# Optimization experiments

Hardware: AMD Instinct MI355X
Metric: run time of the kernel (lower is better)

## Reference

```python
import jax, jax.numpy as jnp
import numpy as np
import math
from jax import lax

B, L = 64, 8192
S = L // 8          # width after 3 stride-(1,2) SAME convs
D = 4 * 5           # height(4) * channels(5) -> per-token feature dim
D_FLAT = S * D


def setup_inputs():
    key = jax.random.key(0)
    ks = jax.random.split(key, 32)
    sc = 0.1
    inp = {
        "inputs": jax.random.randint(ks[0], (B, L), 0, 4, dtype=jnp.int32),
        # conv stack: HWIO kernels, Conv2D(5,(4,4),(1,2),'SAME')
        "conv_w1": sc * jax.random.normal(ks[1], (4, 4, 1, 5), jnp.float32),
        "conv_b1": jnp.zeros((5,), jnp.float32),
        "conv_w2": sc * jax.random.normal(ks[2], (4, 4, 5, 5), jnp.float32),
        "conv_b2": jnp.zeros((5,), jnp.float32),
        "conv_w3": sc * jax.random.normal(ks[3], (4, 4, 5, 5), jnp.float32),
        "conv_b3": jnp.zeros((5,), jnp.float32),
        # 3 SelfAttn blocks, each with K/Q/V projections [D, D]
        "attn1_K": sc * jax.random.normal(ks[4], (D, D), jnp.float32),
        "attn1_Q": sc * jax.random.normal(ks[5], (D, D), jnp.float32),
        "attn1_V": sc * jax.random.normal(ks[6], (D, D), jnp.float32),
        "attn2_K": sc * jax.random.normal(ks[7], (D, D), jnp.float32),
        "attn2_Q": sc * jax.random.normal(ks[8], (D, D), jnp.float32),
        "attn2_V": sc * jax.random.normal(ks[9], (D, D), jnp.float32),
        "attn3_K": sc * jax.random.normal(ks[10], (D, D), jnp.float32),
        "attn3_Q": sc * jax.random.normal(ks[11], (D, D), jnp.float32),
        "attn3_V": sc * jax.random.normal(ks[12], (D, D), jnp.float32),
        # 3 Dense(10) layers (no activation, as in Keras defaults)
        "dense_w1": 0.01 * jax.random.normal(ks[13], (D_FLAT, 10), jnp.float32),
        "dense_b1": jnp.zeros((10,), jnp.float32),
        "dense_w2": sc * jax.random.normal(ks[14], (10, 10), jnp.float32),
        "dense_b2": jnp.zeros((10,), jnp.float32),
        "dense_w3": sc * jax.random.normal(ks[15], (10, 10), jnp.float32),
        "dense_b3": jnp.zeros((10,), jnp.float32),
    }
    return inp


def _conv(x, w, b):
    # NHWC, HWIO, strides (1,2), SAME
    y = lax.conv_general_dilated(x, w, window_strides=(1, 2), padding="SAME",
                                 dimension_numbers=("NHWC", "HWIO", "NHWC"))
    return y + b


def _self_attn(x, Kw, Qw, Vw):
    # x: [B, S, D]; manual causal scaled dot-product attention
    K = x @ Kw
    Q = x @ Qw
    V = x @ Vw
    s = Q.shape[1]
    mask = jnp.triu(jnp.full((s, s), -jnp.inf, dtype=x.dtype), k=1)
    scores = jnp.einsum("bsd,btd->bst", Q, K) / math.sqrt(K.shape[-1]) + mask
    return jax.nn.softmax(scores, axis=-1) @ V


def reference(inputs, conv_w1, conv_b1, conv_w2, conv_b2, conv_w3, conv_b3,
              attn1_K, attn1_Q, attn1_V, attn2_K, attn2_Q, attn2_V,
              attn3_K, attn3_Q, attn3_V,
              dense_w1, dense_b1, dense_w2, dense_b2, dense_w3, dense_b3):
    # one_hot over axis=1 -> [B, 4, L], then channel dim -> [B, 4, L, 1]
    x = jax.nn.one_hot(inputs, 4, axis=1, dtype=jnp.float32)[..., None]
    x = _conv(x, conv_w1, conv_b1)
    x = _conv(x, conv_w2, conv_b2)
    x = _conv(x, conv_w3, conv_b3)            # [B, 4, S, 5]
    # tokens along width, features = height(4) x channels(5)
    x = jnp.transpose(x, (0, 2, 1, 3)).reshape(x.shape[0], S, D)
    x = _self_attn(x, attn1_K, attn1_Q, attn1_V)
    x = _self_attn(x, attn2_K, attn2_Q, attn2_V)
    x = _self_attn(x, attn3_K, attn3_Q, attn3_V)
    x = x.reshape(x.shape[0], -1)             # flatten [B, S*D]
    x = x @ dense_w1 + dense_b1
    x = x @ dense_w2 + dense_b2
    x = x @ dense_w3 + dense_b3               # [B, 10]
    return x
```

## Files before the change

kernel.cpp:

```cpp
#include <hip/hip_runtime.h>
#include <hip/hip_bf16.h>


#define B_ 64
#define L_ 8192
#define S_ 1024
#define D_ 20

typedef unsigned short ushort_t;
typedef __attribute__((ext_vector_type(8))) short short8_t;
typedef __attribute__((ext_vector_type(4))) short short4_t;
typedef __attribute__((ext_vector_type(4))) float f32x4_t;

__device__ __forceinline__ ushort_t f2bf(float f) {
  unsigned u = __float_as_uint(f);
  return (ushort_t)((u + 0x7fffu + ((u >> 16) & 1u)) >> 16);
}
__device__ __forceinline__ float bf2f(ushort_t h) {
  return __uint_as_float(((unsigned)h) << 16);
}

__global__ __launch_bounds__(256) void conv12_kernel(
    const int* __restrict__ inp,
    const float* __restrict__ W1c, const float* __restrict__ B1c,
    const float* __restrict__ W2c, const float* __restrict__ B2c,
    float* __restrict__ out,
    const float* __restrict__ W1d,
    float* __restrict__ W1T) {
  __shared__ float w1s[80], b1s[5], w2s[400], b2s[5];
  for (int j = threadIdx.x; j < 400; j += 256) w2s[j] = W2c[j];
  if (threadIdx.x < 80)      w1s[threadIdx.x]      = W1c[threadIdx.x];
  else if (threadIdx.x < 85) b1s[threadIdx.x - 80] = B1c[threadIdx.x - 80];
  else if (threadIdx.x < 90) b2s[threadIdx.x - 85] = B2c[threadIdx.x - 85];
  __syncthreads();
  const int idx = blockIdx.x * 256 + threadIdx.x;
  const int b  = idx >> 11;
  const int wo = idx & 2047;
  const int* ib = inp + (size_t)b * L_;
  int iv[10];
#pragma unroll
  for (int t = 0; t < 10; ++t) {
    int g = 4 * wo - 3 + t;
    iv[t] = (g >= 0 && g < L_) ? ib[g] : -100;
  }
  float val[4][4][5];
#pragma unroll
  for (int pos = 0; pos < 4; ++pos) {
    const int w1 = 2 * wo - 1 + pos;
    const bool okp = (w1 >= 0 && w1 < 4096);
#pragma unroll
    for (int hi = 0; hi < 4; ++hi)
#pragma unroll
      for (int ci = 0; ci < 5; ++ci) val[hi][pos][ci] = okp ? b1s[ci] : 0.f;
    if (okp) {
#pragma unroll
      for (int kw = 0; kw < 4; ++kw) {
        const int gw = 2 * w1 - 1 + kw;
        if (gw >= 0 && gw < L_) {
          const int v = iv[2 * pos + kw];
#pragma unroll
          for (int hi = 0; hi < 4; ++hi) {
            const int kh = v - hi + 1;
            if (kh >= 0 && kh < 4) {
#pragma unroll
              for (int ci = 0; ci < 5; ++ci)
                val[hi][pos][ci] += w1s[(kh * 4 + kw) * 5 + ci];
            }
          }
        }
      }
    }
  }
  float acc[4][5];
#pragma unroll
  for (int h = 0; h < 4; ++h)
#pragma unroll
    for (int c = 0; c < 5; ++c) acc[h][c] = b2s[c];
#pragma unroll
  for (int kh = 0; kh < 4; ++kh)
#pragma unroll
    for (int kw = 0; kw < 4; ++kw)
#pragma unroll
      for (int ci = 0; ci < 5; ++ci) {
        const float* wp = w2s + ((kh * 4 + kw) * 5 + ci) * 5;
        float w0 = wp[0], w1v = wp[1], w2v = wp[2], w3 = wp[3], w4 = wp[4];
#pragma unroll
        for (int h = 0; h < 4; ++h) {
          int hi = h - 1 + kh;
          if (hi >= 0 && hi < 4) {
            float x = val[hi][kw][ci];
            acc[h][0] += w0 * x;  acc[h][1] += w1v * x; acc[h][2] += w2v * x;
            acc[h][3] += w3 * x;  acc[h][4] += w4 * x;
          }
        }
      }
  float* ob = out + (size_t)b * 4 * 2048 * 5;
#pragma unroll
  for (int h = 0; h < 4; ++h)
#pragma unroll
    for (int c = 0; c < 5; ++c) ob[(h * 2048 + wo) * 5 + c] = acc[h][c];
  for (int j = idx; j < 204800; j += 131072) {
    int col = j / 20480, i2 = j - col * 20480;
    W1T[j] = W1d[i2 * 10 + col];
  }
}

__global__ __launch_bounds__(256) void conv3_proj_kernel(
    const float* __restrict__ in,
    const float* __restrict__ W,  const float* __restrict__ Bi,
    const float* __restrict__ Kw, const float* __restrict__ Qw,
    const float* __restrict__ Vw,
    ushort_t* __restrict__ Qb, ushort_t* __restrict__ Kb,
    ushort_t* __restrict__ Vf) {
  constexpr int WIN = 2048;
  __shared__ float ws[400], bs[5];
  __shared__ float kw[400], qw[400], vw[400];
  for (int j = threadIdx.x; j < 400; j += 256) {
    ws[j] = W[j]; kw[j] = Kw[j]; qw[j] = Qw[j]; vw[j] = Vw[j];
  }
  if (threadIdx.x < 5) bs[threadIdx.x] = Bi[threadIdx.x];
  __syncthreads();
  const int r  = blockIdx.x * 256 + threadIdx.x;
  const int b  = r >> 10;
  const int wo = r & 1023;
  float val[4][4][5];
#pragma unroll
  for (int hi = 0; hi < 4; ++hi) {
    const float* ir = in + ((size_t)b * 4 + hi) * WIN * 5;
#pragma unroll
    for (int kwp = 0; kwp < 4; ++kwp) {
      int wi = 2 * wo - 1 + kwp;
      bool ok = (wi >= 0 && wi < WIN);
#pragma unroll
      for (int ci = 0; ci < 5; ++ci) val[hi][kwp][ci] = ok ? ir[wi * 5 + ci] : 0.f;
    }
  }
  float acc[4][5];
#pragma unroll
  for (int h = 0; h < 4; ++h)
#pragma unroll
    for (int c = 0; c < 5; ++c) acc[h][c] = bs[c];
#pragma unroll
  for (int kh = 0; kh < 4; ++kh)
#pragma unroll
    for (int kwp = 0; kwp < 4; ++kwp)
#pragma unroll
      for (int ci = 0; ci < 5; ++ci) {
        const float* wp = ws + ((kh * 4 + kwp) * 5 + ci) * 5;
        float w0 = wp[0], w1 = wp[1], w2 = wp[2], w3 = wp[3], w4 = wp[4];
#pragma unroll
        for (int h = 0; h < 4; ++h) {
          int hi = h - 1 + kh;
          if (hi >= 0 && hi < 4) {
            float x = val[hi][kwp][ci];
            acc[h][0] += w0 * x; acc[h][1] += w1 * x; acc[h][2] += w2 * x;
            acc[h][3] += w3 * x; acc[h][4] += w4 * x;
          }
        }
      }
  float x[D_];
#pragma unroll
  for (int h = 0; h < 4; ++h)
#pragma unroll
    for (int c = 0; c < 5; ++c) x[h * 5 + c] = acc[h][c];
  float q[D_], k[D_], v[D_];
#pragma unroll
  for (int j = 0; j < D_; ++j) { q[j] = 0.f; k[j] = 0.f; v[j] = 0.f; }
#pragma unroll
  for (int i = 0; i < D_; ++i) {
#pragma unroll
    for (int j = 0; j < D_; ++j) {
      q[j] += x[i] * qw[i * D_ + j];
      k[j] += x[i] * kw[i * D_ + j];
      v[j] += x[i] * vw[i * D_ + j];
    }
  }
  const float sc = 0.22360679774997896f;
  ushort_t qt[32], kt[32];
#pragma unroll
  for (int j = 0; j < D_; ++j) { qt[j] = f2bf(q[j] * sc); kt[j] = f2bf(k[j]); }
#pragma unroll
  for (int j = D_; j < 32; ++j) { qt[j] = 0; kt[j] = 0; }
  int4* qd = (int4*)(Qb + (size_t)r * 32);
  int4* kd = (int4*)(Kb + (size_t)r * 32);
#pragma unroll
  for (int j = 0; j < 4; ++j) {
    qd[j] = *(const int4*)(qt + 8 * j);
    kd[j] = *(const int4*)(kt + 8 * j);
  }
  ushort_t* vbase = Vf + ((size_t)b * 64 + (wo >> 4)) * 320 + (wo & 15);
#pragma unroll
  for (int d = 0; d < D_; ++d) vbase[d * 16] = f2bf(v[d]);
}

template <bool FUSE>
__global__ __launch_bounds__(512, 8) void attn_kernel(
    const ushort_t* __restrict__ Qb, const ushort_t* __restrict__ Kb,
    const ushort_t* __restrict__ Vf,
    const float* __restrict__ Kw2, const float* __restrict__ Qw2,
    const float* __restrict__ Vw2,
    ushort_t* __restrict__ Qb2, ushort_t* __restrict__ Kb2,
    ushort_t* __restrict__ Vf2,
    const float* __restrict__ W1T,
    float* __restrict__ part2) {
  __shared__ float ox[1280];
  __shared__ float pw_s[FUSE ? 1200 : 4];
  __shared__ float mrgL[64];
  __shared__ float red2[40];
  const int blk   = blockIdx.x;
  const int b     = blk & 63;
  const int raw   = blk >> 6;
  const int rr4   = raw & 3, k4 = raw >> 2;
  const int strip = (k4 == 0) ? rr4 : (k4 == 1) ? 7 - rr4
                  : (k4 == 2) ? 8 + rr4 : 15 - rr4;
  const int q0    = strip * 64;
  const int nt    = q0 + 64;
  const int tid   = threadIdx.x;
  const int w     = tid >> 6;
  const int sub   = w & 3;
  const int half  = w >> 2;
  const int lane  = tid & 63;
  const int n     = lane & 15;
  const int quad  = lane >> 4;
  const int qbase = q0 + 16 * sub;
  const int qg    = qbase + n;
  if (FUSE) {
    for (int j = tid; j < 1200; j += 512) {
      int m = j / 400, oo = j - m * 400;
      pw_s[j] = (m == 0) ? Kw2[oo] : (m == 1) ? Qw2[oo] : Vw2[oo];
    }
  }
  const ushort_t* KbB  = Kb + (size_t)b * 1024 * 32;
  const ushort_t* VfB  = Vf + (size_t)b * 20480;
  const ushort_t* vloB = VfB + n * 16 + quad * 4;
  const ushort_t* vhiB = VfB + (16 + (n & 3)) * 16 + quad * 4;
  short8_t qfrag = *(const short8_t*)(Qb + ((size_t)(b * 1024 + qbase + n)) * 32 + quad * 8);
  f32x4_t oA = {0.f, 0.f, 0.f, 0.f};
  f32x4_t oB = {0.f, 0.f, 0.f, 0.f};
  const f32x4_t zero = {0.f, 0.f, 0.f, 0.f};
  float lsum = 0.f;
  const int nt2 = nt >> 1;
  const int tlo = half ? nt2 : 0;
  int thi = half ? nt : nt2;
  if (thi > qbase + 16) thi = qbase + 16;
  for (int t0 = tlo; t0 < thi; t0 += 32) {
    short8_t kf0 = *(const short8_t*)(KbB + (size_t)(t0 + n) * 32 + quad * 8);
    short8_t kf1 = *(const short8_t*)(KbB + (size_t)(t0 + 16 + n) * 32 + quad * 8);
#pragma unroll
    for (int c = 0; c < 2; ++c) {
      const int tg = t0 + c * 16 + quad * 4;
      f32x4_t s = __builtin_amdgcn_mfma_f32_16x16x32_bf16(c ? kf1 : kf0, qfrag,
                                                          zero, 0, 0, 0);
      ushort_t pk4[4];
#pragma unroll
      for (int r = 0; r < 4; ++r) {
        float p = (tg + r <= qg) ? __expf(s[r]) : 0.f;
        ushort_t h = f2bf(p);
        lsum += bf2f(h);
        pk4[r] = h;
      }
      short4_t pfrag = *(const short4_t*)pk4;
      const int tb = (t0 >> 4) + c;
      short4_t vlo = *(const short4_t*)(vloB + tb * 320);
      short4_t vhi = *(const short4_t*)(vhiB + tb * 320);
      oA = __builtin_amdgcn_mfma_f32_16x16x16bf16_1k(vlo, pfrag, oA, 0, 0, 0);
      oB = __builtin_amdgcn_mfma_f32_16x16x16bf16_1k(vhi, pfrag, oB, 0, 0, 0);
    }
  }
  float l = lsum;
  l += __shfl_xor(l, 16, 64);
  l += __shfl_xor(l, 32, 64);
  float* oxw = ox + sub * 320;
  if (half) {
#pragma unroll
    for (int r = 0; r < 4; ++r) oxw[n * 20 + quad * 4 + r] = oA[r];
    if (quad == 0) {
#pragma unroll
      for (int r = 0; r < 4; ++r) oxw[n * 20 + 16 + r] = oB[r];
      mrgL[sub * 16 + n] = l;
    }
  }
  __syncthreads();
  if (!half) {
#pragma unroll
    for (int r = 0; r < 4; ++r) oA[r] += oxw[n * 20 + quad * 4 + r];
    if (quad == 0) {
#pragma unroll
      for (int r = 0; r < 4; ++r) oB[r] += oxw[n * 20 + 16 + r];
    }
    l += mrgL[sub * 16 + n];
    const float inv = 1.f / l;
#pragma unroll
    for (int r = 0; r < 4; ++r) oxw[n * 20 + quad * 4 + r] = oA[r] * inv;
    if (quad == 0) {
#pragma unroll
      for (int r = 0; r < 4; ++r) oxw[n * 20 + 16 + r] = oB[r] * inv;
    }
  }
  if (FUSE) {
    if (!half) {
      __asm__ volatile("s_waitcnt lgkmcnt(0)" ::: "memory");
      const int row  = lane >> 2;
      const int part = lane & 3;
      float x[D_];
#pragma unroll
      for (int i = 0; i < D_; ++i) x[i] = oxw[row * 20 + i];
      float qv[5], kv[5], vv[5];
#pragma unroll
      for (int jj = 0; jj < 5; ++jj) { qv[jj] = 0.f; kv[jj] = 0.f; vv[jj] = 0.f; }
#pragma unroll
      for (int i = 0; i < D_; ++i) {
        const float xi = x[i];
#pragma unroll
        for (int jj = 0; jj < 5; ++jj) {
          const int j = 5 * part + jj;
          kv[jj] += xi * pw_s[i * 20 + j];
          qv[jj] += xi * pw_s[400 + i * 20 + j];
          vv[jj] += xi * pw_s[800 + i * 20 + j];
        }
      }
      const float sc = 0.22360679774997896f;
      const int rg = b * 1024 + qbase + row;
      const int s  = rg & 1023;
#pragma unroll
      for (int jj = 0; jj < 5; ++jj) {
        const int j = 5 * part + jj;
        Kb2[(size_t)rg * 32 + j] = f2bf(kv[jj]);
        Qb2[(size_t)rg * 32 + j] = f2bf(qv[jj] * sc);
        Vf2[(size_t)b * 20480 + (size_t)(s >> 4) * 320 + j * 16 + (s & 15)] =
            f2bf(vv[jj]);
      }
      if (part == 0) {
#pragma unroll
        for (int u = 0; u < 6; ++u)
          *(unsigned*)(Kb2 + (size_t)rg * 32 + 20 + 2 * u) = 0u;
      } else if (part == 1) {
#pragma unroll
        for (int u = 0; u < 6; ++u)
          *(unsigned*)(Qb2 + (size_t)rg * 32 + 20 + 2 * u) = 0u;
      }
    }
  } else {
    __syncthreads();
    float acc[10];
#pragma unroll
    for (int j = 0; j < 10; ++j) acc[j] = 0.f;
    const int base = q0 * 20;
    if (tid < 256) {
#pragma unroll
      for (int k = 0; k < 5; ++k) {
        const int il = tid + 256 * k;
        const float xv = ox[il];
#pragma unroll
        for (int j = 0; j < 10; ++j)
          acc[j] += xv * W1T[(size_t)j * 20480 + base + il];
      }
    }
#pragma unroll
    for (int off = 1; off < 64; off <<= 1) {
#pragma unroll
      for (int j = 0; j < 10; ++j) acc[j] += __shfl_xor(acc[j], off, 64);
    }
    if (tid < 256 && lane == 0) {
#pragma unroll
      for (int j = 0; j < 10; ++j) red2[w * 10 + j] = acc[j];
    }
    __syncthreads();
    if (tid < 10) {
      float s2 = red2[tid] + red2[10 + tid] + red2[20 + tid] + red2[30 + tid];
      part2[((b << 4) + strip) * 10 + tid] = s2;
    }
  }
}

__global__ __launch_bounds__(64) void dense_final(
    const float* __restrict__ part2,
    const float* __restrict__ B1,
    const float* __restrict__ W2, const float* __restrict__ B2,
    const float* __restrict__ W3, const float* __restrict__ B3,
    float* __restrict__ out) {
  const int b = blockIdx.x;
  __shared__ float y1[10], y2[10];
  if (threadIdx.x < 10) {
    int j = threadIdx.x;
    float s = 0.f;
#pragma unroll
    for (int st = 0; st < 16; ++st) s += part2[((b << 4) + st) * 10 + j];
    y1[j] = s + B1[j];
  }
  __syncthreads();
  if (threadIdx.x < 10) {
    int j = threadIdx.x;
    float s = B2[j];
#pragma unroll
    for (int i = 0; i < 10; ++i) s += y1[i] * W2[i * 10 + j];
    y2[j] = s;
  }
  __syncthreads();
  if (threadIdx.x < 10) {
    int j = threadIdx.x;
    float s = B3[j];
#pragma unroll
    for (int i = 0; i < 10; ++i) s += y2[i] * W3[i * 10 + j];
    out[b * 10 + j] = s;
  }
}

extern "C" void kernel_launch(void* const* d_in, const int* in_sizes, int n_in,
                              void* d_out, int out_size, void* d_ws, size_t ws_size,
                              hipStream_t stream) {
  const int*   inp = (const int*)d_in[0];
  const float* cw1 = (const float*)d_in[1];
  const float* cb1 = (const float*)d_in[2];
  const float* cw2 = (const float*)d_in[3];
  const float* cb2 = (const float*)d_in[4];
  const float* cw3 = (const float*)d_in[5];
  const float* cb3 = (const float*)d_in[6];
  const float* a1K = (const float*)d_in[7];
  const float* a1Q = (const float*)d_in[8];
  const float* a1V = (const float*)d_in[9];
  const float* a2K = (const float*)d_in[10];
  const float* a2Q = (const float*)d_in[11];
  const float* a2V = (const float*)d_in[12];
  const float* a3K = (const float*)d_in[13];
  const float* a3Q = (const float*)d_in[14];
  const float* a3V = (const float*)d_in[15];
  const float* dw1 = (const float*)d_in[16];
  const float* db1 = (const float*)d_in[17];
  const float* dw2 = (const float*)d_in[18];
  const float* db2 = (const float*)d_in[19];
  const float* dw3 = (const float*)d_in[20];
  const float* db3 = (const float*)d_in[21];
  float* outp = (float*)d_out;

  float* wsf = (float*)d_ws;
  ushort_t* qbA  = (ushort_t*)(wsf);
  ushort_t* kbA  = (ushort_t*)(wsf + 1048576);
  ushort_t* vfA  = (ushort_t*)(wsf + 2097152);
  float*    part2= wsf + 4456448;
  float*    w1t  = wsf + 4466688;
  ushort_t* qbB  = (ushort_t*)(wsf + 4671488);
  ushort_t* kbB  = (ushort_t*)(wsf + 5712384);
  ushort_t* vfB  = (ushort_t*)(wsf + 6760960);
  float*    c2   = wsf + 5242880;

  conv12_kernel<<<512, 256, 0, stream>>>(inp, cw1, cb1, cw2, cb2, c2, dw1, w1t);

  conv3_proj_kernel<<<256, 256, 0, stream>>>(c2, cw3, cb3, a1K, a1Q, a1V, qbA, kbA, vfA);
  attn_kernel<true><<<1024, 512, 0, stream>>>(
      qbA, kbA, vfA, a2K, a2Q, a2V, qbB, kbB, vfB, nullptr, nullptr);
  attn_kernel<true><<<1024, 512, 0, stream>>>(
      qbB, kbB, vfB, a3K, a3Q, a3V, qbA, kbA, vfA, nullptr, nullptr);
  attn_kernel<false><<<1024, 512, 0, stream>>>(
      qbA, kbA, vfA, nullptr, nullptr, nullptr, nullptr, nullptr, nullptr,
      w1t, part2);

  dense_final<<<64, 64, 0, stream>>>(part2, db1, dw2, db2, dw3, db3, outp);
}
```

Measured before the change: 199.2 us.

## Split conv kernels across four lanes per output with shuffle reduction

Result: no change. 202.0 us (+1.4%).

```diff
diff --git a/kernel.cpp b/kernel.cpp
--- a/kernel.cpp
+++ b/kernel.cpp
@@ -33,75 +33,71 @@
   else if (threadIdx.x < 85) b1s[threadIdx.x - 80] = B1c[threadIdx.x - 80];
   else if (threadIdx.x < 90) b2s[threadIdx.x - 85] = B2c[threadIdx.x - 85];
   __syncthreads();
-  const int idx = blockIdx.x * 256 + threadIdx.x;
-  const int b  = idx >> 11;
-  const int wo = idx & 2047;
+  const int j   = blockIdx.x * 256 + threadIdx.x;
+  const int pos = j & 3;
+  const int idx = j >> 2;
+  const int b   = idx >> 11;
+  const int wo  = idx & 2047;
   const int* ib = inp + (size_t)b * L_;
-  int iv[10];
-#pragma unroll
-  for (int t = 0; t < 10; ++t) {
-    int g = 4 * wo - 3 + t;
-    iv[t] = (g >= 0 && g < L_) ? ib[g] : -100;
-  }
-  float val[4][4][5];
-#pragma unroll
-  for (int pos = 0; pos < 4; ++pos) {
-    const int w1 = 2 * wo - 1 + pos;
-    const bool okp = (w1 >= 0 && w1 < 4096);
-#pragma unroll
-    for (int hi = 0; hi < 4; ++hi)
-#pragma unroll
-      for (int ci = 0; ci < 5; ++ci) val[hi][pos][ci] = okp ? b1s[ci] : 0.f;
-    if (okp) {
-#pragma unroll
-      for (int kw = 0; kw < 4; ++kw) {
-        const int gw = 2 * w1 - 1 + kw;
-        if (gw >= 0 && gw < L_) {
-          const int v = iv[2 * pos + kw];
-#pragma unroll
-          for (int hi = 0; hi < 4; ++hi) {
-            const int kh = v - hi + 1;
-            if (kh >= 0 && kh < 4) {
-#pragma unroll
-              for (int ci = 0; ci < 5; ++ci)
-                val[hi][pos][ci] += w1s[(kh * 4 + kw) * 5 + ci];
-            }
+  float vp[4][5];
+  const int w1 = 2 * wo - 1 + pos;
+  const bool okp = (w1 >= 0 && w1 < 4096);
+#pragma unroll
+  for (int hi = 0; hi < 4; ++hi)
+#pragma unroll
+    for (int ci = 0; ci < 5; ++ci) vp[hi][ci] = okp ? b1s[ci] : 0.f;
+  if (okp) {
+#pragma unroll
+    for (int kw = 0; kw < 4; ++kw) {
+      const int gw = 2 * w1 - 1 + kw;
+      if (gw >= 0 && gw < L_) {
+        const int v = ib[gw];
+#pragma unroll
+        for (int hi = 0; hi < 4; ++hi) {
+          const int kh = v - hi + 1;
+          if (kh >= 0 && kh < 4) {
+#pragma unroll
+            for (int ci = 0; ci < 5; ++ci)
+              vp[hi][ci] += w1s[(kh * 4 + kw) * 5 + ci];
           }
         }
       }
     }
   }
-  float acc[4][5];
+  float part[4][5];
 #pragma unroll
   for (int h = 0; h < 4; ++h)
 #pragma unroll
-    for (int c = 0; c < 5; ++c) acc[h][c] = b2s[c];
+    for (int c = 0; c < 5; ++c) part[h][c] = 0.f;
 #pragma unroll
   for (int kh = 0; kh < 4; ++kh)
 #pragma unroll
-    for (int kw = 0; kw < 4; ++kw)
-#pragma unroll
-      for (int ci = 0; ci < 5; ++ci) {
-        const float* wp = w2s + ((kh * 4 + kw) * 5 + ci) * 5;
-        float w0 = wp[0], w1v = wp[1], w2v = wp[2], w3 = wp[3], w4 = wp[4];
-#pragma unroll
-        for (int h = 0; h < 4; ++h) {
-          int hi = h - 1 + kh;
-          if (hi >= 0 && hi < 4) {
-            float x = val[hi][kw][ci];
-            acc[h][0] += w0 * x;  acc[h][1] += w1v * x; acc[h][2] += w2v * x;
-            acc[h][3] += w3 * x;  acc[h][4] += w4 * x;
-          }
+    for (int ci = 0; ci < 5; ++ci) {
+      const float* wp = w2s + ((kh * 4 + pos) * 5 + ci) * 5;
+      float w0 = wp[0], w1v = wp[1], w2v = wp[2], w3v = wp[3], w4v = wp[4];
+#pragma unroll
+      for (int h = 0; h < 4; ++h) {
+        int hi = h - 1 + kh;
+        if (hi >= 0 && hi < 4) {
+          float x = vp[hi][ci];
+          part[h][0] += w0 * x;  part[h][1] += w1v * x; part[h][2] += w2v * x;
+          part[h][3] += w3v * x; part[h][4] += w4v * x;
         }
       }
+    }
+#pragma unroll
+  for (int m = 1; m <= 2; m <<= 1)
+#pragma unroll
+    for (int h = 0; h < 4; ++h)
+#pragma unroll
+      for (int c = 0; c < 5; ++c) part[h][c] += __shfl_xor(part[h][c], m, 64);
   float* ob = out + (size_t)b * 4 * 2048 * 5;
 #pragma unroll
-  for (int h = 0; h < 4; ++h)
-#pragma unroll
-    for (int c = 0; c < 5; ++c) ob[(h * 2048 + wo) * 5 + c] = acc[h][c];
-  for (int j = idx; j < 204800; j += 131072) {
-    int col = j / 20480, i2 = j - col * 20480;
-    W1T[j] = W1d[i2 * 10 + col];
+  for (int c = 0; c < 5; ++c)
+    ob[(pos * 2048 + wo) * 5 + c] = part[pos][c] + b2s[c];
+  for (int t = j; t < 204800; t += 524288) {
+    int col = t / 20480, i2 = t - col * 20480;
+    W1T[t] = W1d[i2 * 10 + col];
   }
 }
 
@@ -114,83 +110,90 @@
     ushort_t* __restrict__ Vf) {
   constexpr int WIN = 2048;
   __shared__ float ws[400], bs[5];
-  __shared__ float kw[400], qw[400], vw[400];
-  for (int j = threadIdx.x; j < 400; j += 256) {
-    ws[j] = W[j]; kw[j] = Kw[j]; qw[j] = Qw[j]; vw[j] = Vw[j];
+  __shared__ float kws[400], qws[400], vws[400];
+  for (int i = threadIdx.x; i < 400; i += 256) {
+    ws[i] = W[i]; kws[i] = Kw[i]; qws[i] = Qw[i]; vws[i] = Vw[i];
   }
   if (threadIdx.x < 5) bs[threadIdx.x] = Bi[threadIdx.x];
   __syncthreads();
-  const int r  = blockIdx.x * 256 + threadIdx.x;
+  const int j  = blockIdx.x * 256 + threadIdx.x;
+  const int p  = j & 3;
+  const int r  = j >> 2;
   const int b  = r >> 10;
   const int wo = r & 1023;
-  float val[4][4][5];
+  const int wi = 2 * wo - 1 + p;
+  const bool ok = (wi >= 0 && wi < WIN);
+  float vp[4][5];
 #pragma unroll
   for (int hi = 0; hi < 4; ++hi) {
     const float* ir = in + ((size_t)b * 4 + hi) * WIN * 5;
 #pragma unroll
-    for (int kwp = 0; kwp < 4; ++kwp) {
-      int wi = 2 * wo - 1 + kwp;
-      bool ok = (wi >= 0 && wi < WIN);
-#pragma unroll
-      for (int ci = 0; ci < 5; ++ci) val[hi][kwp][ci] = ok ? ir[wi * 5 + ci] : 0.f;
-    }
-  }
-  float acc[4][5];
+    for (int ci = 0; ci < 5; ++ci) vp[hi][ci] = ok ? ir[wi * 5 + ci] : 0.f;
+  }
+  float part[4][5];
 #pragma unroll
   for (int h = 0; h < 4; ++h)
 #pragma unroll
-    for (int c = 0; c < 5; ++c) acc[h][c] = bs[c];
+    for (int c = 0; c < 5; ++c) part[h][c] = 0.f;
 #pragma unroll
   for (int kh = 0; kh < 4; ++kh)
 #pragma unroll
-    for (int kwp = 0; kwp < 4; ++kwp)
-#pragma unroll
-      for (int ci = 0; ci < 5; ++ci) {
-        const float* wp = ws + ((kh * 4 + kwp) * 5 + ci) * 5;
-        float w0 = wp[0], w1 = wp[1], w2 = wp[2], w3 = wp[3], w4 = wp[4];
-#pragma unroll
-        for (int h = 0; h < 4; ++h) {
-          int hi = h - 1 + kh;
-          if (hi >= 0 && hi < 4) {
-            float x = val[hi][kwp][ci];
-            acc[h][0] += w0 * x; acc[h][1] += w1 * x; acc[h][2] += w2 * x;
-            acc[h][3] += w3 * x; acc[h][4] += w4 * x;
-          }
+    for (int ci = 0; ci < 5; ++ci) {
+      const float* wp = ws + ((kh * 4 + p) * 5 + ci) * 5;
+      float w0 = wp[0], w1 = wp[1], w2 = wp[2], w3 = wp[3], w4 = wp[4];
+#pragma unroll
+      for (int h = 0; h < 4; ++h) {
+        int hi = h - 1 + kh;
+        if (hi >= 0 && hi < 4) {
+          float x = vp[hi][ci];
+          part[h][0] += w0 * x; part[h][1] += w1 * x; part[h][2] += w2 * x;
+          part[h][3] += w3 * x; part[h][4] += w4 * x;
         }
       }
+    }
+#pragma unroll
+  for (int m = 1; m <= 2; m <<= 1)
+#pragma unroll
+    for (int h = 0; h < 4; ++h)
+#pragma unroll
+      for (int c = 0; c < 5; ++c) part[h][c] += __shfl_xor(part[h][c], m, 64);
   float x[D_];
 #pragma unroll
   for (int h = 0; h < 4; ++h)
 #pragma unroll
-    for (int c = 0; c < 5; ++c) x[h * 5 + c] = acc[h][c];
-  float q[D_], k[D_], v[D_];
-#pragma unroll
-  for (int j = 0; j < D_; ++j) { q[j] = 0.f; k[j] = 0.f; v[j] = 0.f; }
+    for (int c = 0; c < 5; ++c) x[h * 5 + c] = part[h][c] + bs[c];
+  float qv[5], kv[5], vv[5];
+#pragma unroll
+  for (int jj = 0; jj < 5; ++jj) { qv[jj] = 0.f; kv[jj] = 0.f; vv[jj] = 0.f; }
 #pragma unroll
   for (int i = 0; i < D_; ++i) {
-#pragma unroll
-    for (int j = 0; j < D_; ++j) {
-      q[j] += x[i] * qw[i * D_ + j];
-      k[j] += x[i] * kw[i * D_ + j];
-      v[j] += x[i] * vw[i * D_ + j];
+    const float xi = x[i];
+#pragma unroll
+    for (int jj = 0; jj < 5; ++jj) {
+      const int col = 5 * p + jj;
+      kv[jj] += xi * kws[i * D_ + col];
+      qv[jj] += xi * qws[i * D_ + col];
+      vv[jj] += xi * vws[i * D_ + col];
     }
   }
   const float sc = 0.22360679774997896f;
-  ushort_t qt[32], kt[32];
-#pragma unroll
-  for (int j = 0; j < D_; ++j) { qt[j] = f2bf(q[j] * sc); kt[j] = f2bf(k[j]); }
-#pragma unroll
-  for (int j = D_; j < 32; ++j) { qt[j] = 0; kt[j] = 0; }
-  int4* qd = (int4*)(Qb + (size_t)r * 32);
-  int4* kd = (int4*)(Kb + (size_t)r * 32);
-#pragma unroll
-  for (int j = 0; j < 4; ++j) {
-    qd[j] = *(const int4*)(qt + 8 * j);
-    kd[j] = *(const int4*)(kt + 8 * j);
-  }
-  ushort_t* vbase = Vf + ((size_t)b * 64 + (wo >> 4)) * 320 + (wo & 15);
-#pragma unroll
-  for (int d = 0; d < D_; ++d) vbase[d * 16] = f2bf(v[d]);
+#pragma unroll
+  for (int jj = 0; jj < 5; ++jj) {
+    const int col = 5 * p + jj;
+    Kb[(size_t)r * 32 + col] = f2bf(kv[jj]);
+    Qb[(size_t)r * 32 + col] = f2bf(qv[jj] * sc);
+    Vf[(size_t)b * 20480 + (size_t)(wo >> 4) * 320 + col * 16 + (wo & 15)] =
+        f2bf(vv[jj]);
+  }
+  if (p == 0) {
+#pragma unroll
+    for (int u = 0; u < 6; ++u)
+      *(unsigned*)(Kb + (size_t)r * 32 + 20 + 2 * u) = 0u;
+  } else if (p == 1) {
+#pragma unroll
+    for (int u = 0; u < 6; ++u)
+      *(unsigned*)(Qb + (size_t)r * 32 + 20 + 2 * u) = 0u;
+  }
 }
 
 template <bool FUSE>
@@ -225,9 +228,9 @@
   const int qbase = q0 + 16 * sub;
   const int qg    = qbase + n;
   if (FUSE) {
-    for (int j = tid; j < 1200; j += 512) {
-      int m = j / 400, oo = j - m * 400;
-      pw_s[j] = (m == 0) ? Kw2[oo] : (m == 1) ? Qw2[oo] : Vw2[oo];
+    for (int i = tid; i < 1200; i += 512) {
+      int m = i / 400, oo = i - m * 400;
+      pw_s[i] = (m == 0) ? Kw2[oo] : (m == 1) ? Qw2[oo] : Vw2[oo];
     }
   }
   const ushort_t* KbB  = Kb + (size_t)b * 1024 * 32;
@@ -444,9 +447,9 @@
   ushort_t* vfB  = (ushort_t*)(wsf + 6760960);
   float*    c2   = wsf + 5242880;
 
-  conv12_kernel<<<512, 256, 0, stream>>>(inp, cw1, cb1, cw2, cb2, c2, dw1, w1t);
-
-  conv3_proj_kernel<<<256, 256, 0, stream>>>(c2, cw3, cb3, a1K, a1Q, a1V, qbA, kbA, vfA);
+  conv12_kernel<<<2048, 256, 0, stream>>>(inp, cw1, cb1, cw2, cb2, c2, dw1, w1t);
+
+  conv3_proj_kernel<<<1024, 256, 0, stream>>>(c2, cw3, cb3, a1K, a1Q, a1V, qbA, kbA, vfA);
   attn_kernel<true><<<1024, 512, 0, stream>>>(
       qbA, kbA, vfA, a2K, a2Q, a2V, qbB, kbB, vfB, nullptr, nullptr);
   attn_kernel<true><<<1024, 512, 0, stream>>>(
```

## Split attention into 16-query blocks with 8-wave key-chunk partitioning

Applied to the files above, without the earlier changes.

After: 218.1 us. 1.09x slower.

```diff
diff --git a/kernel.cpp b/kernel.cpp
--- a/kernel.cpp
+++ b/kernel.cpp
@@ -203,108 +203,87 @@
     ushort_t* __restrict__ Vf2,
     const float* __restrict__ W1T,
     float* __restrict__ part2) {
-  __shared__ float ox[1280];
+  __shared__ float oLDS[8][320];
+  __shared__ float lL[8][16];
+  __shared__ float ox[320];
+  __shared__ float linv_s[16];
   __shared__ float pw_s[FUSE ? 1200 : 4];
-  __shared__ float mrgL[64];
-  __shared__ float red2[40];
-  const int blk   = blockIdx.x;
-  const int b     = blk & 63;
-  const int raw   = blk >> 6;
-  const int rr4   = raw & 3, k4 = raw >> 2;
-  const int strip = (k4 == 0) ? rr4 : (k4 == 1) ? 7 - rr4
-                  : (k4 == 2) ? 8 + rr4 : 15 - rr4;
-  const int q0    = strip * 64;
-  const int nt    = q0 + 64;
-  const int tid   = threadIdx.x;
-  const int w     = tid >> 6;
-  const int sub   = w & 3;
-  const int half  = w >> 2;
-  const int lane  = tid & 63;
-  const int n     = lane & 15;
-  const int quad  = lane >> 4;
-  const int qbase = q0 + 16 * sub;
-  const int qg    = qbase + n;
+  __shared__ float red2[FUSE ? 4 : 80];
+  const int blk  = blockIdx.x;
+  const int b    = blk & 63;
+  const int qb   = 63 - (blk >> 6);
+  const int tid  = threadIdx.x;
+  const int h    = tid >> 6;
+  const int lane = tid & 63;
+  const int n    = lane & 15;
+  const int quad = lane >> 4;
+  const int qg   = qb * 16 + n;
   if (FUSE) {
-    for (int j = tid; j < 1200; j += 512) {
-      int m = j / 400, oo = j - m * 400;
-      pw_s[j] = (m == 0) ? Kw2[oo] : (m == 1) ? Qw2[oo] : Vw2[oo];
-    }
-  }
-  const ushort_t* KbB  = Kb + (size_t)b * 1024 * 32;
+    for (int i = tid; i < 1200; i += 512) {
+      int m = i / 400, oo = i - m * 400;
+      pw_s[i] = (m == 0) ? Kw2[oo] : (m == 1) ? Qw2[oo] : Vw2[oo];
+    }
+  }
+  const ushort_t* KbB  = Kb + (size_t)b * 32768;
   const ushort_t* VfB  = Vf + (size_t)b * 20480;
   const ushort_t* vloB = VfB + n * 16 + quad * 4;
   const ushort_t* vhiB = VfB + (16 + (n & 3)) * 16 + quad * 4;
-  short8_t qfrag = *(const short8_t*)(Qb + ((size_t)(b * 1024 + qbase + n)) * 32 + quad * 8);
+  short8_t qfrag = *(const short8_t*)(Qb + ((size_t)(b * 1024 + qb * 16 + n)) * 32 + quad * 8);
   f32x4_t oA = {0.f, 0.f, 0.f, 0.f};
   f32x4_t oB = {0.f, 0.f, 0.f, 0.f};
   const f32x4_t zero = {0.f, 0.f, 0.f, 0.f};
   float lsum = 0.f;
-  const int nt2 = nt >> 1;
-  const int tlo = half ? nt2 : 0;
-  int thi = half ? nt : nt2;
-  if (thi > qbase + 16) thi = qbase + 16;
-  for (int t0 = tlo; t0 < thi; t0 += 32) {
-    short8_t kf0 = *(const short8_t*)(KbB + (size_t)(t0 + n) * 32 + quad * 8);
-    short8_t kf1 = *(const short8_t*)(KbB + (size_t)(t0 + 16 + n) * 32 + quad * 8);
-#pragma unroll
-    for (int c = 0; c < 2; ++c) {
-      const int tg = t0 + c * 16 + quad * 4;
-      f32x4_t s = __builtin_amdgcn_mfma_f32_16x16x32_bf16(c ? kf1 : kf0, qfrag,
-                                                          zero, 0, 0, 0);
-      ushort_t pk4[4];
-#pragma unroll
-      for (int r = 0; r < 4; ++r) {
-        float p = (tg + r <= qg) ? __expf(s[r]) : 0.f;
-        ushort_t h = f2bf(p);
-        lsum += bf2f(h);
-        pk4[r] = h;
-      }
-      short4_t pfrag = *(const short4_t*)pk4;
-      const int tb = (t0 >> 4) + c;
-      short4_t vlo = *(const short4_t*)(vloB + tb * 320);
-      short4_t vhi = *(const short4_t*)(vhiB + tb * 320);
-      oA = __builtin_amdgcn_mfma_f32_16x16x16bf16_1k(vlo, pfrag, oA, 0, 0, 0);
-      oB = __builtin_amdgcn_mfma_f32_16x16x16bf16_1k(vhi, pfrag, oB, 0, 0, 0);
-    }
+  const int nc = qb + 1;
+  for (int c = h; c < nc; c += 8) {
+    short8_t kf = *(const short8_t*)(KbB + (size_t)(c * 16 + n) * 32 + quad * 8);
+    const int tg = c * 16 + quad * 4;
+    f32x4_t s = __builtin_amdgcn_mfma_f32_16x16x32_bf16(kf, qfrag, zero, 0, 0, 0);
+    ushort_t pk4[4];
+#pragma unroll
+    for (int r = 0; r < 4; ++r) {
+      float p = (tg + r <= qg) ? __expf(s[r]) : 0.f;
+      ushort_t hh = f2bf(p);
+      lsum += bf2f(hh);
+      pk4[r] = hh;
+    }
+    short4_t pfrag = *(const short4_t*)pk4;
+    short4_t vlo = *(const short4_t*)(vloB + c * 320);
+    short4_t vhi = *(const short4_t*)(vhiB + c * 320);
+    oA = __builtin_amdgcn_mfma_f32_16x16x16bf16_1k(vlo, pfrag, oA, 0, 0, 0);
+    oB = __builtin_amdgcn_mfma_f32_16x16x16bf16_1k(vhi, pfrag, oB, 0, 0, 0);
   }
   float l = lsum;
   l += __shfl_xor(l, 16, 64);
   l += __shfl_xor(l, 32, 64);
-  float* oxw = ox + sub * 320;
-  if (half) {
-#pragma unroll
-    for (int r = 0; r < 4; ++r) oxw[n * 20 + quad * 4 + r] = oA[r];
-    if (quad == 0) {
-#pragma unroll
-      for (int r = 0; r < 4; ++r) oxw[n * 20 + 16 + r] = oB[r];
-      mrgL[sub * 16 + n] = l;
-    }
-  }
-  __syncthreads();
-  if (!half) {
-#pragma unroll
-    for (int r = 0; r < 4; ++r) oA[r] += oxw[n * 20 + quad * 4 + r];
-    if (quad == 0) {
-#pragma unroll
-      for (int r = 0; r < 4; ++r) oB[r] += oxw[n * 20 + 16 + r];
-    }
-    l += mrgL[sub * 16 + n];
-    const float inv = 1.f / l;
-#pragma unroll
-    for (int r = 0; r < 4; ++r) oxw[n * 20 + quad * 4 + r] = oA[r] * inv;
-    if (quad == 0) {
-#pragma unroll
-      for (int r = 0; r < 4; ++r) oxw[n * 20 + 16 + r] = oB[r] * inv;
-    }
-  }
+#pragma unroll
+  for (int r = 0; r < 4; ++r) oLDS[h][n * 20 + quad * 4 + r] = oA[r];
+  if (quad == 0) {
+#pragma unroll
+    for (int r = 0; r < 4; ++r) oLDS[h][n * 20 + 16 + r] = oB[r];
+    lL[h][n] = l;
+  }
+  __syncthreads();
+  if (tid < 16) {
+    float L = 0.f;
+#pragma unroll
+    for (int k = 0; k < 8; ++k) L += lL[k][tid];
+    linv_s[tid] = 1.f / L;
+  }
+  __syncthreads();
+  if (tid < 320) {
+    float s2 = 0.f;
+#pragma unroll
+    for (int k = 0; k < 8; ++k) s2 += oLDS[k][tid];
+    ox[tid] = s2 * linv_s[tid / 20];
+  }
+  __syncthreads();
   if (FUSE) {
-    if (!half) {
-      __asm__ volatile("s_waitcnt lgkmcnt(0)" ::: "memory");
+    if (tid < 64) {
       const int row  = lane >> 2;
       const int part = lane & 3;
       float x[D_];
 #pragma unroll
-      for (int i = 0; i < D_; ++i) x[i] = oxw[row * 20 + i];
+      for (int i = 0; i < D_; ++i) x[i] = ox[row * 20 + i];
       float qv[5], kv[5], vv[5];
 #pragma unroll
       for (int jj = 0; jj < 5; ++jj) { qv[jj] = 0.f; kv[jj] = 0.f; vv[jj] = 0.f; }
@@ -320,15 +299,13 @@
         }
       }
       const float sc = 0.22360679774997896f;
-      const int rg = b * 1024 + qbase + row;
-      const int s  = rg & 1023;
+      const int rg = b * 1024 + qb * 16 + row;
 #pragma unroll
       for (int jj = 0; jj < 5; ++jj) {
         const int j = 5 * part + jj;
         Kb2[(size_t)rg * 32 + j] = f2bf(kv[jj]);
         Qb2[(size_t)rg * 32 + j] = f2bf(qv[jj] * sc);
-        Vf2[(size_t)b * 20480 + (size_t)(s >> 4) * 320 + j * 16 + (s & 15)] =
-            f2bf(vv[jj]);
+        Vf2[(size_t)b * 20480 + (size_t)qb * 320 + j * 16 + row] = f2bf(vv[jj]);
       }
       if (part == 0) {
 #pragma unroll
@@ -341,34 +318,31 @@
       }
     }
   } else {
-    __syncthreads();
     float acc[10];
 #pragma unroll
     for (int j = 0; j < 10; ++j) acc[j] = 0.f;
-    const int base = q0 * 20;
-    if (tid < 256) {
-#pragma unroll
-      for (int k = 0; k < 5; ++k) {
-        const int il = tid + 256 * k;
-        const float xv = ox[il];
-#pragma unroll
-        for (int j = 0; j < 10; ++j)
-          acc[j] += xv * W1T[(size_t)j * 20480 + base + il];
-      }
+    if (tid < 320) {
+      const float xv = ox[tid];
+      const size_t base = (size_t)qb * 320 + tid;
+#pragma unroll
+      for (int j = 0; j < 10; ++j)
+        acc[j] = xv * W1T[(size_t)j * 20480 + base];
     }
 #pragma unroll
     for (int off = 1; off < 64; off <<= 1) {
 #pragma unroll
       for (int j = 0; j < 10; ++j) acc[j] += __shfl_xor(acc[j], off, 64);
     }
-    if (tid < 256 && lane == 0) {
-#pragma unroll
-      for (int j = 0; j < 10; ++j) red2[w * 10 + j] = acc[j];
+    if (lane == 0) {
+#pragma unroll
+      for (int j = 0; j < 10; ++j) red2[h * 10 + j] = acc[j];
     }
     __syncthreads();
     if (tid < 10) {
-      float s2 = red2[tid] + red2[10 + tid] + red2[20 + tid] + red2[30 + tid];
-      part2[((b << 4) + strip) * 10 + tid] = s2;
+      float s2 = 0.f;
+#pragma unroll
+      for (int k = 0; k < 8; ++k) s2 += red2[k * 10 + tid];
+      part2[((b << 6) + qb) * 10 + tid] = s2;
     }
   }
 }
@@ -385,7 +359,7 @@
     int j = threadIdx.x;
     float s = 0.f;
 #pragma unroll
-    for (int st = 0; st < 16; ++st) s += part2[((b << 4) + st) * 10 + j];
+    for (int st = 0; st < 64; ++st) s += part2[((b << 6) + st) * 10 + j];
     y1[j] = s + B1[j];
   }
   __syncthreads();
@@ -437,7 +411,7 @@
   ushort_t* qbA  = (ushort_t*)(wsf);
   ushort_t* kbA  = (ushort_t*)(wsf + 1048576);
   ushort_t* vfA  = (ushort_t*)(wsf + 2097152);
-  float*    part2= wsf + 4456448;
+  float*    part2= wsf + 3145728;
   float*    w1t  = wsf + 4466688;
   ushort_t* qbB  = (ushort_t*)(wsf + 4671488);
   ushort_t* kbB  = (ushort_t*)(wsf + 5712384);
@@ -447,11 +421,11 @@
   conv12_kernel<<<512, 256, 0, stream>>>(inp, cw1, cb1, cw2, cb2, c2, dw1, w1t);
 
   conv3_proj_kernel<<<256, 256, 0, stream>>>(c2, cw3, cb3, a1K, a1Q, a1V, qbA, kbA, vfA);
-  attn_kernel<true><<<1024, 512, 0, stream>>>(
+  attn_kernel<true><<<4096, 512, 0, stream>>>(
       qbA, kbA, vfA, a2K, a2Q, a2V, qbB, kbB, vfB, nullptr, nullptr);
-  attn_kernel<true><<<1024, 512, 0, stream>>>(
+  attn_kernel<true><<<4096, 512, 0, stream>>>(
       qbB, kbB, vfB, a3K, a3Q, a3V, qbA, kbA, vfA, nullptr, nullptr);
-  attn_kernel<false><<<1024, 512, 0, stream>>>(
+  attn_kernel<false><<<4096, 512, 0, stream>>>(
       qbA, kbA, vfA, nullptr, nullptr, nullptr, nullptr, nullptr, nullptr,
       w1t, part2);
 
```

## Fuse conv1/conv2 into conv3+QKV projection kernel via shared-memory halo

Applied to the files above, without the earlier changes.

Result: slower. 363.1 us (+82.3%).

```diff
diff --git a/kernel.cpp b/kernel.cpp
--- a/kernel.cpp
+++ b/kernel.cpp
@@ -20,133 +20,131 @@
   return __uint_as_float(((unsigned)h) << 16);
 }
 
-__global__ __launch_bounds__(256) void conv12_kernel(
+__global__ __launch_bounds__(256) void conv_fused_kernel(
     const int* __restrict__ inp,
     const float* __restrict__ W1c, const float* __restrict__ B1c,
     const float* __restrict__ W2c, const float* __restrict__ B2c,
-    float* __restrict__ out,
+    const float* __restrict__ W3c, const float* __restrict__ B3c,
+    const float* __restrict__ Kw,  const float* __restrict__ Qw,
+    const float* __restrict__ Vw,
+    ushort_t* __restrict__ Qb, ushort_t* __restrict__ Kb,
+    ushort_t* __restrict__ Vf,
     const float* __restrict__ W1d,
     float* __restrict__ W1T) {
   __shared__ float w1s[80], b1s[5], w2s[400], b2s[5];
-  for (int j = threadIdx.x; j < 400; j += 256) w2s[j] = W2c[j];
-  if (threadIdx.x < 80)      w1s[threadIdx.x]      = W1c[threadIdx.x];
-  else if (threadIdx.x < 85) b1s[threadIdx.x - 80] = B1c[threadIdx.x - 80];
-  else if (threadIdx.x < 90) b2s[threadIdx.x - 85] = B2c[threadIdx.x - 85];
+  __shared__ float ws3[400], bs3[5];
+  __shared__ float kws[400], qws[400], vws[400];
+  __shared__ float c2s[514 * 21];
+  const int tid = threadIdx.x;
+  const int blk = blockIdx.x;
+  for (int i = tid; i < 400; i += 256) {
+    w2s[i] = W2c[i]; ws3[i] = W3c[i];
+    kws[i] = Kw[i];  qws[i] = Qw[i];  vws[i] = Vw[i];
+  }
+  if (tid < 80)       w1s[tid]      = W1c[tid];
+  else if (tid < 85)  b1s[tid - 80] = B1c[tid - 80];
+  else if (tid < 90)  b2s[tid - 85] = B2c[tid - 85];
+  else if (tid < 95)  bs3[tid - 90] = B3c[tid - 90];
   __syncthreads();
-  const int idx = blockIdx.x * 256 + threadIdx.x;
-  const int b  = idx >> 11;
-  const int wo = idx & 2047;
+  const int b   = blk >> 2;
+  const int wo0 = (blk & 3) << 8;
   const int* ib = inp + (size_t)b * L_;
-  int iv[10];
-#pragma unroll
-  for (int t = 0; t < 10; ++t) {
-    int g = 4 * wo - 3 + t;
-    iv[t] = (g >= 0 && g < L_) ? ib[g] : -100;
-  }
-  float val[4][4][5];
-#pragma unroll
-  for (int pos = 0; pos < 4; ++pos) {
-    const int w1 = 2 * wo - 1 + pos;
-    const bool okp = (w1 >= 0 && w1 < 4096);
-#pragma unroll
-    for (int hi = 0; hi < 4; ++hi)
-#pragma unroll
-      for (int ci = 0; ci < 5; ++ci) val[hi][pos][ci] = okp ? b1s[ci] : 0.f;
-    if (okp) {
-#pragma unroll
-      for (int kw = 0; kw < 4; ++kw) {
-        const int gw = 2 * w1 - 1 + kw;
-        if (gw >= 0 && gw < L_) {
-          const int v = iv[2 * pos + kw];
-#pragma unroll
-          for (int hi = 0; hi < 4; ++hi) {
-            const int kh = v - hi + 1;
-            if (kh >= 0 && kh < 4) {
-#pragma unroll
-              for (int ci = 0; ci < 5; ++ci)
-                val[hi][pos][ci] += w1s[(kh * 4 + kw) * 5 + ci];
+  for (int sidx = tid; sidx < 514; sidx += 256) {
+    const int wi = 2 * wo0 - 1 + sidx;
+    float acc[4][5];
+    if (wi >= 0 && wi < 2048) {
+      int iv[10];
+#pragma unroll
+      for (int t = 0; t < 10; ++t) {
+        int g = 4 * wi - 3 + t;
+        iv[t] = (g >= 0 && g < L_) ? ib[g] : -100;
+      }
+      float val[4][4][5];
+#pragma unroll
+      for (int pos = 0; pos < 4; ++pos) {
+        const int w1 = 2 * wi - 1 + pos;
+        const bool okp = (w1 >= 0 && w1 < 4096);
+#pragma unroll
+        for (int hi = 0; hi < 4; ++hi)
+#pragma unroll
+          for (int ci = 0; ci < 5; ++ci) val[hi][pos][ci] = okp ? b1s[ci] : 0.f;
+        if (okp) {
+#pragma unroll
+          for (int kw = 0; kw < 4; ++kw) {
+            const int gw = 2 * w1 - 1 + kw;
+            if (gw >= 0 && gw < L_) {
+              const int v = iv[2 * pos + kw];
+#pragma unroll
+              for (int hi = 0; hi < 4; ++hi) {
+                const int kh = v - hi + 1;
+                if (kh >= 0 && kh < 4) {
+#pragma unroll
+                  for (int ci = 0; ci < 5; ++ci)
+                    val[hi][pos][ci] += w1s[(kh * 4 + kw) * 5 + ci];
+                }
+              }
             }
           }
         }
       }
-    }
+#pragma unroll
+      for (int h = 0; h < 4; ++h)
+#pragma unroll
+        for (int c = 0; c < 5; ++c) acc[h][c] = b2s[c];
+#pragma unroll
+      for (int kh = 0; kh < 4; ++kh)
+#pragma unroll
+        for (int kw = 0; kw < 4; ++kw)
+#pragma unroll
+          for (int ci = 0; ci < 5; ++ci) {
+            const float* wp = w2s + ((kh * 4 + kw) * 5 + ci) * 5;
+            float w0 = wp[0], w1v = wp[1], w2v = wp[2], w3v = wp[3], w4v = wp[4];
+#pragma unroll
+            for (int h = 0; h < 4; ++h) {
+              int hi = h - 1 + kh;
+              if (hi >= 0 && hi < 4) {
+                float x = val[hi][kw][ci];
+                acc[h][0] += w0 * x;  acc[h][1] += w1v * x; acc[h][2] += w2v * x;
+                acc[h][3] += w3v * x; acc[h][4] += w4v * x;
+              }
+            }
+          }
+    } else {
+#pragma unroll
+      for (int h = 0; h < 4; ++h)
+#pragma unroll
+        for (int c = 0; c < 5; ++c) acc[h][c] = 0.f;
+    }
+#pragma unroll
+    for (int h = 0; h < 4; ++h)
+#pragma unroll
+      for (int c = 0; c < 5; ++c) c2s[sidx * 21 + h * 5 + c] = acc[h][c];
+  }
+  __syncthreads();
+  const int wo = wo0 + tid;
+  const int r  = (b << 10) + wo;
+  float val[4][4][5];
+#pragma unroll
+  for (int kwp = 0; kwp < 4; ++kwp) {
+    const int lidx = 2 * tid + kwp;
+#pragma unroll
+    for (int hi = 0; hi < 4; ++hi)
+#pragma unroll
+      for (int ci = 0; ci < 5; ++ci)
+        val[hi][kwp][ci] = c2s[lidx * 21 + hi * 5 + ci];
   }
   float acc[4][5];
 #pragma unroll
   for (int h = 0; h < 4; ++h)
 #pragma unroll
-    for (int c = 0; c < 5; ++c) acc[h][c] = b2s[c];
+    for (int c = 0; c < 5; ++c) acc[h][c] = bs3[c];
 #pragma unroll
   for (int kh = 0; kh < 4; ++kh)
 #pragma unroll
-    for (int kw = 0; kw < 4; ++kw)
+    for (int kwp = 0; kwp < 4; ++kwp)
 #pragma unroll
       for (int ci = 0; ci < 5; ++ci) {
-        const float* wp = w2s + ((kh * 4 + kw) * 5 + ci) * 5;
-        float w0 = wp[0], w1v = wp[1], w2v = wp[2], w3 = wp[3], w4 = wp[4];
-#pragma unroll
-        for (int h = 0; h < 4; ++h) {
-          int hi = h - 1 + kh;
-          if (hi >= 0 && hi < 4) {
-            float x = val[hi][kw][ci];
-            acc[h][0] += w0 * x;  acc[h][1] += w1v * x; acc[h][2] += w2v * x;
-            acc[h][3] += w3 * x;  acc[h][4] += w4 * x;
-          }
-        }
-      }
-  float* ob = out + (size_t)b * 4 * 2048 * 5;
-#pragma unroll
-  for (int h = 0; h < 4; ++h)
-#pragma unroll
-    for (int c = 0; c < 5; ++c) ob[(h * 2048 + wo) * 5 + c] = acc[h][c];
-  for (int j = idx; j < 204800; j += 131072) {
-    int col = j / 20480, i2 = j - col * 20480;
-    W1T[j] = W1d[i2 * 10 + col];
-  }
-}
-
-__global__ __launch_bounds__(256) void conv3_proj_kernel(
-    const float* __restrict__ in,
-    const float* __restrict__ W,  const float* __restrict__ Bi,
-    const float* __restrict__ Kw, const float* __restrict__ Qw,
-    const float* __restrict__ Vw,
-    ushort_t* __restrict__ Qb, ushort_t* __restrict__ Kb,
-    ushort_t* __restrict__ Vf) {
-  constexpr int WIN = 2048;
-  __shared__ float ws[400], bs[5];
-  __shared__ float kw[400], qw[400], vw[400];
-  for (int j = threadIdx.x; j < 400; j += 256) {
-    ws[j] = W[j]; kw[j] = Kw[j]; qw[j] = Qw[j]; vw[j] = Vw[j];
-  }
-  if (threadIdx.x < 5) bs[threadIdx.x] = Bi[threadIdx.x];
-  __syncthreads();
-  const int r  = blockIdx.x * 256 + threadIdx.x;
-  const int b  = r >> 10;
-  const int wo = r & 1023;
-  float val[4][4][5];
-#pragma unroll
-  for (int hi = 0; hi < 4; ++hi) {
-    const float* ir = in + ((size_t)b * 4 + hi) * WIN * 5;
-#pragma unroll
-    for (int kwp = 0; kwp < 4; ++kwp) {
-      int wi = 2 * wo - 1 + kwp;
-      bool ok = (wi >= 0 && wi < WIN);
-#pragma unroll
-      for (int ci = 0; ci < 5; ++ci) val[hi][kwp][ci] = ok ? ir[wi * 5 + ci] : 0.f;
-    }
-  }
-  float acc[4][5];
-#pragma unroll
-  for (int h = 0; h < 4; ++h)
-#pragma unroll
-    for (int c = 0; c < 5; ++c) acc[h][c] = bs[c];
-#pragma unroll
-  for (int kh = 0; kh < 4; ++kh)
-#pragma unroll
-    for (int kwp = 0; kwp < 4; ++kwp)
-#pragma unroll
-      for (int ci = 0; ci < 5; ++ci) {
-        const float* wp = ws + ((kh * 4 + kwp) * 5 + ci) * 5;
+        const float* wp = ws3 + ((kh * 4 + kwp) * 5 + ci) * 5;
         float w0 = wp[0], w1 = wp[1], w2 = wp[2], w3 = wp[3], w4 = wp[4];
 #pragma unroll
         for (int h = 0; h < 4; ++h) {
@@ -170,9 +168,9 @@
   for (int i = 0; i < D_; ++i) {
 #pragma unroll
     for (int j = 0; j < D_; ++j) {
-      q[j] += x[i] * qw[i * D_ + j];
-      k[j] += x[i] * kw[i * D_ + j];
-      v[j] += x[i] * vw[i * D_ + j];
+      q[j] += x[i] * qws[i * D_ + j];
+      k[j] += x[i] * kws[i * D_ + j];
+      v[j] += x[i] * vws[i * D_ + j];
     }
   }
   const float sc = 0.22360679774997896f;
@@ -191,6 +189,10 @@
   ushort_t* vbase = Vf + ((size_t)b * 64 + (wo >> 4)) * 320 + (wo & 15);
 #pragma unroll
   for (int d = 0; d < D_; ++d) vbase[d * 16] = f2bf(v[d]);
+  for (int t2 = blk * 256 + tid; t2 < 204800; t2 += 65536) {
+    int col = t2 / 20480, i2 = t2 - col * 20480;
+    W1T[t2] = W1d[i2 * 10 + col];
+  }
 }
 
 template <bool FUSE>
@@ -225,9 +227,9 @@
   const int qbase = q0 + 16 * sub;
   const int qg    = qbase + n;
   if (FUSE) {
-    for (int j = tid; j < 1200; j += 512) {
-      int m = j / 400, oo = j - m * 400;
-      pw_s[j] = (m == 0) ? Kw2[oo] : (m == 1) ? Qw2[oo] : Vw2[oo];
+    for (int i = tid; i < 1200; i += 512) {
+      int m = i / 400, oo = i - m * 400;
+      pw_s[i] = (m == 0) ? Kw2[oo] : (m == 1) ? Qw2[oo] : Vw2[oo];
     }
   }
   const ushort_t* KbB  = Kb + (size_t)b * 1024 * 32;
@@ -442,11 +444,10 @@
   ushort_t* qbB  = (ushort_t*)(wsf + 4671488);
   ushort_t* kbB  = (ushort_t*)(wsf + 5712384);
   ushort_t* vfB  = (ushort_t*)(wsf + 6760960);
-  float*    c2   = wsf + 5242880;
-
-  conv12_kernel<<<512, 256, 0, stream>>>(inp, cw1, cb1, cw2, cb2, c2, dw1, w1t);
-
-  conv3_proj_kernel<<<256, 256, 0, stream>>>(c2, cw3, cb3, a1K, a1Q, a1V, qbA, kbA, vfA);
+
+  conv_fused_kernel<<<256, 256, 0, stream>>>(
+      inp, cw1, cb1, cw2, cb2, cw3, cb3, a1K, a1Q, a1V, qbA, kbA, vfA,
+      dw1, w1t);
   attn_kernel<true><<<1024, 512, 0, stream>>>(
       qbA, kbA, vfA, a2K, a2Q, a2V, qbB, kbB, vfB, nullptr, nullptr);
   attn_kernel<true><<<1024, 512, 0, stream>>>(
```
